# Optimization experiments

Measured on AMD Instinct MI355X. Metric: run time of the kernel, lower is better.

## Reference

```python
import jax, jax.numpy as jnp
import numpy as np
from jax import lax

B, T, J, C = 256, 512, 25, 3
IN_DIM = J * C  # 75
H = 256


def gru_layer(x, W_ih, W_hh, b_ih, b_hh):
    """PyTorch-semantics GRU layer. x: [B,T,Din] -> (out [B,T,H], h_T [B,H]).
    Gate order in stacked weights: r, z, n (PyTorch convention)."""
    Hh = W_hh.shape[1]
    # precompute input contributions for all timesteps
    xg = jnp.einsum('bti,gi->btg', x, W_ih) + b_ih  # [B,T,3H]

    def step(h, xg_t):
        hg = h @ W_hh.T + b_hh  # [B,3H]
        xr, xz, xn = jnp.split(xg_t, 3, axis=-1)
        hr, hz, hn = jnp.split(hg, 3, axis=-1)
        r = jax.nn.sigmoid(xr + hr)
        z = jax.nn.sigmoid(xz + hz)
        n = jnp.tanh(xn + r * hn)
        h_new = (1.0 - z) * n + z * h
        return h_new, h_new

    h0 = jnp.zeros((x.shape[0], Hh), x.dtype)
    hT, outs = lax.scan(step, h0, jnp.swapaxes(xg, 0, 1))  # scan over time
    return jnp.swapaxes(outs, 0, 1), hT


def setup_inputs() -> dict:
    key = jax.random.key(0)
    ks = jax.random.split(key, 12)
    s_in = 1.0 / np.sqrt(H)

    def u(k, shape):
        return jax.random.uniform(k, shape, jnp.float32, -s_in, s_in)

    return {
        'x': jax.random.normal(ks[0], (B, T, J, C), jnp.float32),
        'W_ih0': u(ks[1], (3 * H, IN_DIM)),
        'W_hh0': u(ks[2], (3 * H, H)),
        'b_ih0': u(ks[3], (3 * H,)),
        'b_hh0': u(ks[4], (3 * H,)),
        'W_ih1': u(ks[5], (3 * H, H)),
        'W_hh1': u(ks[6], (3 * H, H)),
        'b_ih1': u(ks[7], (3 * H,)),
        'b_hh1': u(ks[8], (3 * H,)),
        'fc_W': u(ks[9], (H, H)),
        'fc_b': u(ks[10], (H,)),
    }


def reference(x, W_ih0, W_hh0, b_ih0, b_hh0, W_ih1, W_hh1, b_ih1, b_hh1, fc_W, fc_b):
    b, t, j, c = x.shape
    xf = x.reshape(b, t, j * 3)  # matches torch view(B, T, J*3)
    out0, _ = gru_layer(xf, W_ih0, W_hh0, b_ih0, b_hh0)
    _, hT = gru_layer(out0, W_ih1, W_hh1, b_ih1, b_hh1)
    # unidirectional: final hidden state of last layer -> fc
    embedding = hT @ fc_W.T + fc_b  # [B, H]
    return embedding
```

## Files before the change

kernel.cpp:

```cpp
#include <hip/hip_runtime.h>
#include <hip/hip_bf16.h>
#include <stdint.h>
#include <stddef.h>


typedef _Float16 f16;
typedef _Float16 f16x8 __attribute__((ext_vector_type(8)));
typedef _Float16 f16x4 __attribute__((ext_vector_type(4)));
typedef float    f32x4 __attribute__((ext_vector_type(4)));

#define B_      256
#define T_      512
#define H_      256
#define G_      768
#define IN_RAW  75
#define KX      96
#define MROWS   (T_*B_)

__device__ __forceinline__ float rcp_(float x){ return __builtin_amdgcn_rcpf(x); }
__device__ __forceinline__ float sigm(float x){ return rcp_(1.f + __expf(-x)); }
__device__ __forceinline__ float tanh_(float x){ return 1.f - 2.f*rcp_(1.f + __expf(2.f*x)); }

__device__ __forceinline__ void bar_lds(){
  asm volatile("s_waitcnt lgkmcnt(0)" ::: "memory");
  __builtin_amdgcn_s_barrier();
  __builtin_amdgcn_sched_barrier(0);
}

__global__ __launch_bounds__(256) void cast_x(const float* __restrict__ x,
                                              f16* __restrict__ xb){
  int idx = blockIdx.x*256 + threadIdx.x;
  int row = idx / KX;
  int j   = idx - row*KX;
  int t   = row >> 8;
  int b   = row & 255;
  float v = (j < IN_RAW) ? x[((size_t)b*T_ + t)*IN_RAW + j] : 0.f;
  xb[idx] = (f16)v;
}

__global__ __launch_bounds__(256) void cast_w(
    const float* __restrict__ Wih0, const float* __restrict__ Whh0,
    const float* __restrict__ Wih1, const float* __restrict__ Whh1,
    const float* __restrict__ fcW,
    const float* __restrict__ bih0, const float* __restrict__ bhh0,
    const float* __restrict__ bih1, const float* __restrict__ bhh1,
    f16* __restrict__ W0h, f16* __restrict__ Whh0h, f16* __restrict__ Wih1h,
    f16* __restrict__ Whh1h, f16* __restrict__ fcWh,
    float* __restrict__ bias0, float* __restrict__ bias1){
  int i = blockIdx.x*256 + threadIdx.x;
  if (i < 73728){ int r = i/KX, j = i - r*KX;
    W0h[i] = (f16)((j < IN_RAW) ? Wih0[r*IN_RAW + j] : 0.f); return; }
  i -= 73728;
  if (i < 196608){ Whh0h[i] = (f16)Whh0[i]; return; } i -= 196608;
  if (i < 196608){ Wih1h[i] = (f16)Wih1[i]; return; } i -= 196608;
  if (i < 196608){ Whh1h[i] = (f16)Whh1[i]; return; } i -= 196608;
  if (i < 65536){ fcWh[i] = (f16)fcW[i]; return; } i -= 65536;
  if (i < 768){ bias0[i] = bih0[i] + (i < 512 ? bhh0[i] : 0.f); return; } i -= 768;
  if (i < 768){ bias1[i] = bih1[i] + (i < 512 ? bhh1[i] : 0.f); }
}

__global__ __launch_bounds__(256) void cast_h(const float* __restrict__ hs,
                                              f16* __restrict__ hT){
  int i = blockIdx.x*256 + threadIdx.x;
  hT[i] = (f16)hs[i];
}

template<int K, int BN, bool OUTF32>
__global__ __launch_bounds__(256, 2) void gemm_k(const f16* __restrict__ A,
    const f16* __restrict__ W, const float* __restrict__ bias,
    void* __restrict__ outp, const int N){
  constexpr int NT = BN/16;
  const int tid  = threadIdx.x;
  const int wave = tid >> 6, lane = tid & 63;
  const int quad = lane >> 4, l16 = lane & 15;
  const long mbase = (long)blockIdx.x*128 + wave*32;
  const int  nbase = blockIdx.y*BN;
  f32x4 acc[2][NT] = {};
#pragma unroll 2
  for (int kc = 0; kc < K/32; ++kc){
    f16x8 a0 = *(const f16x8*)(A + (mbase +      l16)*K + kc*32 + quad*8);
    f16x8 a1 = *(const f16x8*)(A + (mbase + 16 + l16)*K + kc*32 + quad*8);
#pragma unroll
    for (int nt = 0; nt < NT; ++nt){
      f16x8 b = *(const f16x8*)(W + (long)(nbase + nt*16 + l16)*K + kc*32 + quad*8);
      acc[0][nt] = __builtin_amdgcn_mfma_f32_16x16x32_f16(a0, b, acc[0][nt], 0, 0, 0);
      acc[1][nt] = __builtin_amdgcn_mfma_f32_16x16x32_f16(a1, b, acc[1][nt], 0, 0, 0);
    }
  }
#pragma unroll
  for (int nt = 0; nt < NT; ++nt){
    const int col = nbase + nt*16 + l16;
    const float bv = bias[col];
#pragma unroll
    for (int af = 0; af < 2; ++af){
#pragma unroll
      for (int r = 0; r < 4; ++r){
        const long row = mbase + af*16 + quad*4 + r;
        float v = acc[af][nt][r] + bv;
        if (OUTF32) ((float*)outp)[row*(long)N + col] = v;
        else        ((f16*)outp)[row*(long)N + col] = (f16)v;
      }
    }
  }
}

template<int K>
__device__ __forceinline__ void gemm_body128(const f16* __restrict__ A,
    const f16* __restrict__ W, const float* __restrict__ bias,
    f16* __restrict__ out, const int bx, const int by){
  const int tid  = threadIdx.x;
  const int wave = tid >> 6, lane = tid & 63;
  const int quad = lane >> 4, l16 = lane & 15;
  const int nbase = by*128;
#pragma unroll
  for (int mt = 0; mt < 2; ++mt){
    const long mbase = (long)bx*512 + mt*256 + wave*32;
    f32x4 acc[2][8] = {};
#pragma unroll 2
    for (int kc = 0; kc < K/32; ++kc){
      f16x8 a0 = *(const f16x8*)(A + (mbase +      l16)*K + kc*32 + quad*8);
      f16x8 a1 = *(const f16x8*)(A + (mbase + 16 + l16)*K + kc*32 + quad*8);
#pragma unroll
      for (int nt = 0; nt < 8; ++nt){
        f16x8 b = *(const f16x8*)(W + (long)(nbase + nt*16 + l16)*K + kc*32 + quad*8);
        acc[0][nt] = __builtin_amdgcn_mfma_f32_16x16x32_f16(a0, b, acc[0][nt], 0, 0, 0);
        acc[1][nt] = __builtin_amdgcn_mfma_f32_16x16x32_f16(a1, b, acc[1][nt], 0, 0, 0);
      }
    }
#pragma unroll
    for (int nt = 0; nt < 8; ++nt){
      const int col = nbase + nt*16 + l16;
      const float bv = bias[col];
#pragma unroll
      for (int af = 0; af < 2; ++af)
#pragma unroll
        for (int r = 0; r < 4; ++r)
          out[(mbase + af*16 + quad*4 + r)*(long)G_ + col] = (f16)(acc[af][nt][r] + bv);
    }
  }
}

__device__ __forceinline__ void scan_body(const f16* __restrict__ xg,
    const f16* __restrict__ Whh, const float* __restrict__ bhh,
    float* __restrict__ hstate, f16* __restrict__ out0,
    const int TC, const int bx){
  __shared__ char  hbufB[2][16*512];
  __shared__ f16   nlds[65536];
  __shared__ float bnlds[256];
  const int tid  = threadIdx.x;
  const int wave = tid >> 6, lane = tid & 63;
  const int quad = lane >> 4, l16 = lane & 15;
  const int b0   = bx*16;
  const int jj   = wave*32 + quad*4;

  f16x8 w[2][2][8];
#pragma unroll
  for (int s = 0; s < 2; ++s)
#pragma unroll
    for (int g = 0; g < 2; ++g)
#pragma unroll
      for (int kc = 0; kc < 8; ++kc)
        w[s][g][kc] = *(const f16x8*)(Whh + (size_t)(g*256 + wave*32 + s*16 + l16)*H_ + kc*32 + quad*8);
#pragma unroll
  for (int s = 0; s < 2; ++s)
#pragma unroll
    for (int g = 0; g < 2; ++g)
#pragma unroll
      for (int kc = 0; kc < 8; ++kc)
        asm volatile("" : "+a"(w[s][g][kc]));

#pragma unroll
  for (int i = 0; i < 16; ++i){
    const int p  = i*512 + tid;
    const int f  = p >> 6, L = p & 63;
    const int wv = f >> 4, ss = (f >> 3) & 1, kcc = f & 7;
    const int row = 512 + wv*32 + ss*16 + (L & 15);
    const int k   = kcc*32 + (L >> 4)*8;
    *(f16x8*)&nlds[(size_t)p*8] = *(const f16x8*)(Whh + (size_t)row*H_ + k);
  }
  if (tid < 256) bnlds[tid] = bhh[512 + tid];

  f32x4 h[2];
#pragma unroll
  for (int s = 0; s < 2; ++s){
    h[s] = *(const f32x4*)(hstate + (size_t)(b0 + l16)*H_ + jj + s*16);
    f16x4 hh;
#pragma unroll
    for (int r = 0; r < 4; ++r) hh[r] = (f16)h[s][r];
    const int ch = wave*4 + s*2 + (quad>>1);
    *(f16x4*)&hbufB[0][l16*512 + ((ch ^ (l16&7))<<4) + ((quad&1)<<3)] = hh;
  }

  const f16* xgl = xg + (size_t)(b0 + l16)*G_ + jj;
  f16x4 cur[6];
#pragma unroll
  for (int s = 0; s < 2; ++s)
#pragma unroll
    for (int g = 0; g < 3; ++g)
      cur[s*3+g] = *(const f16x4*)(xgl + g*256 + s*16);

  __syncthreads();

  for (int t = 0; t < TC; ++t){
    const int pb = t & 1;
    f32x4 acc[2][3] = {};
#pragma unroll
    for (int kc = 0; kc < 8; ++kc){
      f16x8 hf = *(const f16x8*)&hbufB[pb][l16*512 + ((((kc<<2)|quad) ^ (l16&7))<<4)];
#pragma unroll
      for (int s = 0; s < 2; ++s){
        acc[s][0] = __builtin_amdgcn_mfma_f32_16x16x32_f16(w[s][0][kc], hf, acc[s][0], 0,0,0);
        acc[s][1] = __builtin_amdgcn_mfma_f32_16x16x32_f16(w[s][1][kc], hf, acc[s][1], 0,0,0);
        f16x8 nf = *(const f16x8*)&nlds[(size_t)(((wave<<4)|(s<<3)|kc)*64 + lane)*8];
        acc[s][2] = __builtin_amdgcn_mfma_f32_16x16x32_f16(nf, hf, acc[s][2], 0,0,0);
      }
    }
    f16x4 hh[2];
#pragma unroll
    for (int s = 0; s < 2; ++s){
      const f32x4 bnv = *(const f32x4*)&bnlds[jj + s*16];
#pragma unroll
      for (int r = 0; r < 4; ++r){
        float rg = sigm((float)cur[s*3+0][r] + acc[s][0][r]);
        float zg = sigm((float)cur[s*3+1][r] + acc[s][1][r]);
        float ng = tanh_((float)cur[s*3+2][r] + rg*(acc[s][2][r] + bnv[r]));
        float hv = (1.f - zg)*ng + zg*h[s][r];
        h[s][r] = hv;
        hh[s][r] = (f16)hv;
      }
    }
    if (t+1 < TC){
      const f16* xn_ = xgl + (size_t)(t+1)*(B_*G_);
#pragma unroll
      for (int s = 0; s < 2; ++s)
#pragma unroll
        for (int g = 0; g < 3; ++g)
          cur[s*3+g] = *(const f16x4*)(xn_ + g*256 + s*16);
    }
#pragma unroll
    for (int s = 0; s < 2; ++s){
      const int ch = wave*4 + s*2 + (quad>>1);
      *(f16x4*)&hbufB[pb^1][l16*512 + ((ch ^ (l16&7))<<4) + ((quad&1)<<3)] = hh[s];
      if (out0)
        *(f16x4*)(out0 + ((size_t)t*B_ + b0 + l16)*H_ + jj + s*16) = hh[s];
    }
    bar_lds();
  }

#pragma unroll
  for (int s = 0; s < 2; ++s)
    *(f32x4*)(hstate + (size_t)(b0 + l16)*H_ + jj + s*16) = h[s];
}

__global__ __launch_bounds__(512)
__attribute__((amdgpu_waves_per_eu(2, 2)))
void fused(
    const f16* __restrict__ xg0, const f16* __restrict__ Whh0,
    const float* __restrict__ bhh0, float* __restrict__ h0s,
    f16* __restrict__ out0w,
    const f16* __restrict__ xg1, const f16* __restrict__ Whh1,
    const float* __restrict__ bhh1, float* __restrict__ h1s,
    const f16* __restrict__ g0A, const f16* __restrict__ g0W,
    const float* __restrict__ g0b, f16* __restrict__ g0out,
    const f16* __restrict__ g1A, const f16* __restrict__ g1W,
    const float* __restrict__ g1b, f16* __restrict__ g1out,
    const int TC, const int mask){
  const int bid = blockIdx.x;
  if (bid < 16){
    if (!(mask & 1)) return;
    scan_body(xg0, Whh0, bhh0, h0s, out0w, TC, bid);
  } else if (bid < 32){
    if (!(mask & 2)) return;
    scan_body(xg1, Whh1, bhh1, h1s, (f16*)nullptr, TC, bid - 16);
  } else {
    int g = bid - 32;
    const int RB = TC/2;
    if (g < 3*TC){
      if (!(mask & 4)) return;
      gemm_body128<96>(g0A, g0W, g0b, g0out, g % RB, g / RB);
    } else {
      g -= 3*TC;
      if (!(mask & 8)) return;
      gemm_body128<256>(g1A, g1W, g1b, g1out, g % RB, g / RB);
    }
  }
}

extern "C" void kernel_launch(void* const* d_in, const int* in_sizes, int n_in,
                              void* d_out, int out_size, void* d_ws, size_t ws_size,
                              hipStream_t stream){
  (void)in_sizes; (void)n_in; (void)out_size;
  const float* x    = (const float*)d_in[0];
  const float* Wih0 = (const float*)d_in[1];
  const float* Whh0 = (const float*)d_in[2];
  const float* bih0 = (const float*)d_in[3];
  const float* bhh0 = (const float*)d_in[4];
  const float* Wih1 = (const float*)d_in[5];
  const float* Whh1 = (const float*)d_in[6];
  const float* bih1 = (const float*)d_in[7];
  const float* bhh1 = (const float*)d_in[8];
  const float* fcW  = (const float*)d_in[9];
  const float* fcb  = (const float*)d_in[10];

  char* ws = (char*)d_ws;
  size_t off = 0;
  auto alloc = [&](size_t bytes) -> void* {
    void* p = ws + off; off += (bytes + 255) & ~(size_t)255; return p;
  };
  f16*   xb    = (f16*)  alloc((size_t)MROWS*KX*2);
  f16*   W0h   = (f16*)  alloc((size_t)G_*KX*2);
  f16*   Whh0h = (f16*)  alloc((size_t)G_*H_*2);
  f16*   Wih1h = (f16*)  alloc((size_t)G_*H_*2);
  f16*   Whh1h = (f16*)  alloc((size_t)G_*H_*2);
  f16*   fcWh  = (f16*)  alloc((size_t)H_*H_*2);
  float* bias0 = (float*)alloc(G_*4);
  float* bias1 = (float*)alloc(G_*4);
  float* h0s   = (float*)alloc((size_t)B_*H_*4);
  float* h1s   = (float*)alloc((size_t)B_*H_*4);
  f16*   hTh   = (f16*)  alloc((size_t)B_*H_*2);
  const size_t fixed = off;

  int TC = 32;
  while (TC > 8 && fixed + (size_t)TC*1835008 + 1024 > ws_size) TC >>= 1;
  f16* xg0[2], *xg1[2], *out0[2];
  xg0[0]  = (f16*)alloc((size_t)TC*B_*G_*2);
  xg0[1]  = (f16*)alloc((size_t)TC*B_*G_*2);
  xg1[0]  = (f16*)alloc((size_t)TC*B_*G_*2);
  xg1[1]  = (f16*)alloc((size_t)TC*B_*G_*2);
  out0[0] = (f16*)alloc((size_t)TC*B_*H_*2);
  out0[1] = (f16*)alloc((size_t)TC*B_*H_*2);
  const int nc = T_ / TC;

  hipMemsetAsync(h0s, 0, (size_t)B_*H_*4*2, stream);
  hipLaunchKernelGGL(cast_x, dim3(49152), dim3(256), 0, stream, x, xb);
  hipLaunchKernelGGL(cast_w, dim3(2854), dim3(256), 0, stream,
                     Wih0, Whh0, Wih1, Whh1, fcW, bih0, bhh0, bih1, bhh1,
                     W0h, Whh0h, Wih1h, Whh1h, fcWh, bias0, bias1);

  hipLaunchKernelGGL((gemm_k<96,192,false>), dim3(TC*2,4), dim3(256), 0, stream,
                     xb, W0h, bias0, (void*)xg0[0], G_);

  const dim3 grid(32 + 6*TC);
  for (int i = 0; i <= nc + 1; ++i){
    int mask = 0;
    if (i < nc)            mask |= 1;
    if (i >= 2)            mask |= 2;
    if (i + 1 < nc)        mask |= 4;
    if (i >= 1 && i <= nc) mask |= 8;
    hipLaunchKernelGGL(fused, grid, dim3(512), 0, stream,
                       xg0[i&1], Whh0h, bhh0, h0s, out0[i&1],
                       xg1[i&1], Whh1h, bhh1, h1s,
                       xb + (size_t)(i+1)*TC*B_*KX, W0h, bias0, xg0[(i+1)&1],
                       out0[(i+1)&1], Wih1h, bias1, xg1[(i+1)&1],
                       TC, mask);
  }

  hipLaunchKernelGGL(cast_h, dim3(256), dim3(256), 0, stream, h1s, hTh);
  hipLaunchKernelGGL((gemm_k<256,64,true>), dim3(2,4), dim3(256), 0, stream,
                     hTh, fcWh, fcb, d_out, H_);
}
```

Measured before the change: 1.688 ms.

## Hold all recurrent weights in registers with 4-wave scan blocks

```diff
diff --git a/kernel.cpp b/kernel.cpp
--- a/kernel.cpp
+++ b/kernel.cpp
@@ -105,30 +105,30 @@
 }
 
 template<int K>
-__device__ __forceinline__ void gemm_body128(const f16* __restrict__ A,
+__device__ __forceinline__ void gemm_body4(const f16* __restrict__ A,
     const f16* __restrict__ W, const float* __restrict__ bias,
     f16* __restrict__ out, const int bx, const int by){
   const int tid  = threadIdx.x;
   const int wave = tid >> 6, lane = tid & 63;
   const int quad = lane >> 4, l16 = lane & 15;
-  const int nbase = by*128;
+  const int nbase = by*384;
 #pragma unroll
   for (int mt = 0; mt < 2; ++mt){
-    const long mbase = (long)bx*512 + mt*256 + wave*32;
-    f32x4 acc[2][8] = {};
-#pragma unroll 2
+    const long mbase = (long)bx*256 + mt*128 + wave*32;
+    f32x4 acc[2][24] = {};
+#pragma unroll 1
     for (int kc = 0; kc < K/32; ++kc){
       f16x8 a0 = *(const f16x8*)(A + (mbase +      l16)*K + kc*32 + quad*8);
       f16x8 a1 = *(const f16x8*)(A + (mbase + 16 + l16)*K + kc*32 + quad*8);
 #pragma unroll
-      for (int nt = 0; nt < 8; ++nt){
+      for (int nt = 0; nt < 24; ++nt){
         f16x8 b = *(const f16x8*)(W + (long)(nbase + nt*16 + l16)*K + kc*32 + quad*8);
         acc[0][nt] = __builtin_amdgcn_mfma_f32_16x16x32_f16(a0, b, acc[0][nt], 0, 0, 0);
         acc[1][nt] = __builtin_amdgcn_mfma_f32_16x16x32_f16(a1, b, acc[1][nt], 0, 0, 0);
       }
     }
 #pragma unroll
-    for (int nt = 0; nt < 8; ++nt){
+    for (int nt = 0; nt < 24; ++nt){
       const int col = nbase + nt*16 + l16;
       const float bv = bias[col];
 #pragma unroll
@@ -144,116 +144,111 @@
     const f16* __restrict__ Whh, const float* __restrict__ bhh,
     float* __restrict__ hstate, f16* __restrict__ out0,
     const int TC, const int bx){
-  __shared__ char  hbufB[2][16*512];
-  __shared__ f16   nlds[65536];
+  __shared__ char  hbufB[2][8192];
   __shared__ float bnlds[256];
   const int tid  = threadIdx.x;
   const int wave = tid >> 6, lane = tid & 63;
   const int quad = lane >> 4, l16 = lane & 15;
   const int b0   = bx*16;
-  const int jj   = wave*32 + quad*4;
-
-  f16x8 w[2][2][8];
-#pragma unroll
-  for (int s = 0; s < 2; ++s)
-#pragma unroll
-    for (int g = 0; g < 2; ++g)
-#pragma unroll
-      for (int kc = 0; kc < 8; ++kc)
-        w[s][g][kc] = *(const f16x8*)(Whh + (size_t)(g*256 + wave*32 + s*16 + l16)*H_ + kc*32 + quad*8);
-#pragma unroll
-  for (int s = 0; s < 2; ++s)
-#pragma unroll
-    for (int g = 0; g < 2; ++g)
-#pragma unroll
-      for (int kc = 0; kc < 8; ++kc)
-        asm volatile("" : "+a"(w[s][g][kc]));
-
-#pragma unroll
-  for (int i = 0; i < 16; ++i){
-    const int p  = i*512 + tid;
-    const int f  = p >> 6, L = p & 63;
-    const int wv = f >> 4, ss = (f >> 3) & 1, kcc = f & 7;
-    const int row = 512 + wv*32 + ss*16 + (L & 15);
-    const int k   = kcc*32 + (L >> 4)*8;
-    *(f16x8*)&nlds[(size_t)p*8] = *(const f16x8*)(Whh + (size_t)row*H_ + k);
-  }
-  if (tid < 256) bnlds[tid] = bhh[512 + tid];
-
-  f32x4 h[2];
-#pragma unroll
-  for (int s = 0; s < 2; ++s){
+  const int jj   = wave*64 + quad*4;
+
+  f16x8 wz[4][8], wn[4][8], wr[4][8];
+#pragma unroll
+  for (int s = 0; s < 4; ++s)
+#pragma unroll
+    for (int kc = 0; kc < 8; ++kc){
+      wz[s][kc] = *(const f16x8*)(Whh + (size_t)(256 + wave*64 + s*16 + l16)*H_ + kc*32 + quad*8);
+      asm volatile("" : "+a"(wz[s][kc]));
+    }
+#pragma unroll
+  for (int s = 0; s < 4; ++s)
+#pragma unroll
+    for (int kc = 0; kc < 8; ++kc){
+      wn[s][kc] = *(const f16x8*)(Whh + (size_t)(512 + wave*64 + s*16 + l16)*H_ + kc*32 + quad*8);
+      asm volatile("" : "+a"(wn[s][kc]));
+    }
+#pragma unroll
+  for (int s = 0; s < 4; ++s)
+#pragma unroll
+    for (int kc = 0; kc < 8; ++kc){
+      wr[s][kc] = *(const f16x8*)(Whh + (size_t)(wave*64 + s*16 + l16)*H_ + kc*32 + quad*8);
+      asm volatile("" : "+v"(wr[s][kc]));
+    }
+
+  bnlds[tid] = bhh[512 + tid];
+
+  f32x4 h[4];
+#pragma unroll
+  for (int s = 0; s < 4; ++s){
     h[s] = *(const f32x4*)(hstate + (size_t)(b0 + l16)*H_ + jj + s*16);
     f16x4 hh;
 #pragma unroll
     for (int r = 0; r < 4; ++r) hh[r] = (f16)h[s][r];
-    const int ch = wave*4 + s*2 + (quad>>1);
+    const int ch = wave*8 + s*2 + (quad>>1);
     *(f16x4*)&hbufB[0][l16*512 + ((ch ^ (l16&7))<<4) + ((quad&1)<<3)] = hh;
   }
 
   const f16* xgl = xg + (size_t)(b0 + l16)*G_ + jj;
-  f16x4 cur[6];
-#pragma unroll
-  for (int s = 0; s < 2; ++s)
+  f16* o0l = out0 ? out0 + (size_t)(b0 + l16)*H_ + jj : (f16*)nullptr;
+  f16x4 cur[12];
+#pragma unroll
+  for (int s = 0; s < 4; ++s)
 #pragma unroll
     for (int g = 0; g < 3; ++g)
       cur[s*3+g] = *(const f16x4*)(xgl + g*256 + s*16);
 
   __syncthreads();
 
+#pragma unroll 1
   for (int t = 0; t < TC; ++t){
     const int pb = t & 1;
-    f32x4 acc[2][3] = {};
+    f32x4 accR[4] = {}, accZ[4] = {}, accN[4] = {};
 #pragma unroll
     for (int kc = 0; kc < 8; ++kc){
       f16x8 hf = *(const f16x8*)&hbufB[pb][l16*512 + ((((kc<<2)|quad) ^ (l16&7))<<4)];
 #pragma unroll
-      for (int s = 0; s < 2; ++s){
-        acc[s][0] = __builtin_amdgcn_mfma_f32_16x16x32_f16(w[s][0][kc], hf, acc[s][0], 0,0,0);
-        acc[s][1] = __builtin_amdgcn_mfma_f32_16x16x32_f16(w[s][1][kc], hf, acc[s][1], 0,0,0);
-        f16x8 nf = *(const f16x8*)&nlds[(size_t)(((wave<<4)|(s<<3)|kc)*64 + lane)*8];
-        acc[s][2] = __builtin_amdgcn_mfma_f32_16x16x32_f16(nf, hf, acc[s][2], 0,0,0);
+      for (int s = 0; s < 4; ++s){
+        accR[s] = __builtin_amdgcn_mfma_f32_16x16x32_f16(wr[s][kc], hf, accR[s], 0,0,0);
+        accZ[s] = __builtin_amdgcn_mfma_f32_16x16x32_f16(wz[s][kc], hf, accZ[s], 0,0,0);
+        accN[s] = __builtin_amdgcn_mfma_f32_16x16x32_f16(wn[s][kc], hf, accN[s], 0,0,0);
       }
     }
-    f16x4 hh[2];
-#pragma unroll
-    for (int s = 0; s < 2; ++s){
+#pragma unroll
+    for (int s = 0; s < 4; ++s){
       const f32x4 bnv = *(const f32x4*)&bnlds[jj + s*16];
+      f16x4 hh;
 #pragma unroll
       for (int r = 0; r < 4; ++r){
-        float rg = sigm((float)cur[s*3+0][r] + acc[s][0][r]);
-        float zg = sigm((float)cur[s*3+1][r] + acc[s][1][r]);
-        float ng = tanh_((float)cur[s*3+2][r] + rg*(acc[s][2][r] + bnv[r]));
-        float hv = (1.f - zg)*ng + zg*h[s][r];
+        float rg = sigm((float)cur[s*3+0][r] + accR[s][r]);
+        float zg = sigm((float)cur[s*3+1][r] + accZ[s][r]);
+        float ng = tanh_((float)cur[s*3+2][r] + rg*(accN[s][r] + bnv[r]));
+        float hv = ng + zg*(h[s][r] - ng);
         h[s][r] = hv;
-        hh[s][r] = (f16)hv;
+        hh[r]   = (f16)hv;
       }
+      const int ch = wave*8 + s*2 + (quad>>1);
+      *(f16x4*)&hbufB[pb^1][l16*512 + ((ch ^ (l16&7))<<4) + ((quad&1)<<3)] = hh;
+      if (o0l)
+        *(f16x4*)(o0l + (size_t)t*(B_*H_) + s*16) = hh;
     }
     if (t+1 < TC){
       const f16* xn_ = xgl + (size_t)(t+1)*(B_*G_);
 #pragma unroll
-      for (int s = 0; s < 2; ++s)
+      for (int s = 0; s < 4; ++s)
 #pragma unroll
         for (int g = 0; g < 3; ++g)
           cur[s*3+g] = *(const f16x4*)(xn_ + g*256 + s*16);
     }
-#pragma unroll
-    for (int s = 0; s < 2; ++s){
-      const int ch = wave*4 + s*2 + (quad>>1);
-      *(f16x4*)&hbufB[pb^1][l16*512 + ((ch ^ (l16&7))<<4) + ((quad&1)<<3)] = hh[s];
-      if (out0)
-        *(f16x4*)(out0 + ((size_t)t*B_ + b0 + l16)*H_ + jj + s*16) = hh[s];
-    }
     bar_lds();
   }
 
 #pragma unroll
-  for (int s = 0; s < 2; ++s)
+  for (int s = 0; s < 4; ++s)
     *(f32x4*)(hstate + (size_t)(b0 + l16)*H_ + jj + s*16) = h[s];
 }
 
-__global__ __launch_bounds__(512)
-__attribute__((amdgpu_waves_per_eu(2, 2)))
+__global__ __launch_bounds__(256, 1)
+__attribute__((amdgpu_waves_per_eu(1, 1)))
 void fused(
     const f16* __restrict__ xg0, const f16* __restrict__ Whh0,
     const float* __restrict__ bhh0, float* __restrict__ h0s,
@@ -274,14 +269,13 @@
     scan_body(xg1, Whh1, bhh1, h1s, (f16*)nullptr, TC, bid - 16);
   } else {
     int g = bid - 32;
-    const int RB = TC/2;
-    if (g < 3*TC){
+    if (g < 2*TC){
       if (!(mask & 4)) return;
-      gemm_body128<96>(g0A, g0W, g0b, g0out, g % RB, g / RB);
+      gemm_body4<96>(g0A, g0W, g0b, g0out, g % TC, g / TC);
     } else {
-      g -= 3*TC;
+      g -= 2*TC;
       if (!(mask & 8)) return;
-      gemm_body128<256>(g1A, g1W, g1b, g1out, g % RB, g / RB);
+      gemm_body4<256>(g1A, g1W, g1b, g1out, g % TC, g / TC);
     }
   }
 }
@@ -340,14 +334,14 @@
   hipLaunchKernelGGL((gemm_k<96,192,false>), dim3(TC*2,4), dim3(256), 0, stream,
                      xb, W0h, bias0, (void*)xg0[0], G_);
 
-  const dim3 grid(32 + 6*TC);
+  const dim3 grid(32 + 4*TC);
   for (int i = 0; i <= nc + 1; ++i){
     int mask = 0;
     if (i < nc)            mask |= 1;
     if (i >= 2)            mask |= 2;
     if (i + 1 < nc)        mask |= 4;
     if (i >= 1 && i <= nc) mask |= 8;
-    hipLaunchKernelGGL(fused, grid, dim3(512), 0, stream,
+    hipLaunchKernelGGL(fused, grid, dim3(256), 0, stream,
                        xg0[i&1], Whh0h, bhh0, h0s, out0[i&1],
                        xg1[i&1], Whh1h, bhh1, h1s,
                        xb + (size_t)(i+1)*TC*B_*KX, W0h, bias0, xg0[(i+1)&1],
```

Result: slower. 2.816 ms (+66.9%).

## Replace per-chunk kernel launches with one persistent cooperative kernel using grid sync

Applied to the files above, without the earlier changes.

```diff
diff --git a/kernel.cpp b/kernel.cpp
--- a/kernel.cpp
+++ b/kernel.cpp
@@ -1,7 +1,10 @@
 #include <hip/hip_runtime.h>
 #include <hip/hip_bf16.h>
+#include <hip/hip_cooperative_groups.h>
 #include <stdint.h>
 #include <stddef.h>
+
+namespace cg = cooperative_groups;
 
 
 typedef _Float16 f16;
@@ -144,7 +147,7 @@
     const f16* __restrict__ Whh, const float* __restrict__ bhh,
     float* __restrict__ hstate, f16* __restrict__ out0,
     const int TC, const int bx){
-  __shared__ char  hbufB[2][16*512];
+  __shared__ char  hbufB[2][8192];
   __shared__ f16   nlds[65536];
   __shared__ float bnlds[256];
   const int tid  = threadIdx.x;
@@ -286,6 +289,156 @@
   }
 }
 
+__global__ __launch_bounds__(512)
+__attribute__((amdgpu_waves_per_eu(2, 2)))
+void fusedP(const f16* __restrict__ xb,
+            const f16* __restrict__ W0h, const float* __restrict__ bias0,
+            const f16* __restrict__ Whh0h, const float* __restrict__ bhh0,
+            const f16* __restrict__ Wih1h, const float* __restrict__ bias1,
+            const f16* __restrict__ Whh1h, const float* __restrict__ bhh1,
+            float* __restrict__ h1s,
+            f16* __restrict__ xg0a, f16* __restrict__ xg0b,
+            f16* __restrict__ xg1a, f16* __restrict__ xg1b,
+            f16* __restrict__ out0a, f16* __restrict__ out0b,
+            const int TC, const int nc){
+  cg::grid_group gg = cg::this_grid();
+  const int bid = blockIdx.x;
+  if (bid < 32){
+    __shared__ char  hbufB[2][8192];
+    __shared__ f16   nlds[65536];
+    __shared__ float bnlds[256];
+    const bool L1w = bid >= 16;
+    const f16*   Whh = L1w ? Whh1h : Whh0h;
+    const float* bhh = L1w ? bhh1  : bhh0;
+    const int tid  = threadIdx.x;
+    const int wave = tid >> 6, lane = tid & 63;
+    const int quad = lane >> 4, l16 = lane & 15;
+    const int b0   = (bid & 15)*16;
+    const int jj   = wave*32 + quad*4;
+
+    f16x8 w[2][2][8];
+#pragma unroll
+    for (int s = 0; s < 2; ++s)
+#pragma unroll
+      for (int g = 0; g < 2; ++g)
+#pragma unroll
+        for (int kc = 0; kc < 8; ++kc)
+          w[s][g][kc] = *(const f16x8*)(Whh + (size_t)(g*256 + wave*32 + s*16 + l16)*H_ + kc*32 + quad*8);
+#pragma unroll
+    for (int s = 0; s < 2; ++s)
+#pragma unroll
+      for (int g = 0; g < 2; ++g)
+#pragma unroll
+        for (int kc = 0; kc < 8; ++kc)
+          asm volatile("" : "+a"(w[s][g][kc]));
+
+#pragma unroll
+    for (int i = 0; i < 16; ++i){
+      const int p  = i*512 + tid;
+      const int f  = p >> 6, L = p & 63;
+      const int wv = f >> 4, ss = (f >> 3) & 1, kcc = f & 7;
+      const int row = 512 + wv*32 + ss*16 + (L & 15);
+      const int k   = kcc*32 + (L >> 4)*8;
+      *(f16x8*)&nlds[(size_t)p*8] = *(const f16x8*)(Whh + (size_t)row*H_ + k);
+    }
+    if (tid < 256) bnlds[tid] = bhh[512 + tid];
+
+    f32x4 h[2] = {};
+#pragma unroll
+    for (int s = 0; s < 2; ++s){
+      const int ch = wave*4 + s*2 + (quad>>1);
+      *(f16x4*)&hbufB[0][l16*512 + ((ch ^ (l16&7))<<4) + ((quad&1)<<3)] = (f16x4){0,0,0,0};
+    }
+    __syncthreads();
+
+    for (int i = 0; i <= nc + 1; ++i){
+      const int c = L1w ? i - 2 : i;
+      if (c >= 0 && c < nc){
+        const f16* xgc = L1w ? ((c&1) ? xg1b : xg1a) : ((c&1) ? xg0b : xg0a);
+        f16* o0c       = L1w ? (f16*)nullptr        : ((c&1) ? out0b : out0a);
+        const f16* xgl = xgc + (size_t)(b0 + l16)*G_ + jj;
+        f16* o0l = o0c ? o0c + (size_t)(b0 + l16)*H_ + jj : (f16*)nullptr;
+        f16x4 cur[6];
+#pragma unroll
+        for (int s = 0; s < 2; ++s)
+#pragma unroll
+          for (int g = 0; g < 3; ++g)
+            cur[s*3+g] = *(const f16x4*)(xgl + g*256 + s*16);
+
+        for (int t = 0; t < TC; ++t){
+          const int pb = t & 1;
+          f32x4 acc[2][3] = {};
+#pragma unroll
+          for (int kc = 0; kc < 8; ++kc){
+            f16x8 hf = *(const f16x8*)&hbufB[pb][l16*512 + ((((kc<<2)|quad) ^ (l16&7))<<4)];
+#pragma unroll
+            for (int s = 0; s < 2; ++s){
+              acc[s][0] = __builtin_amdgcn_mfma_f32_16x16x32_f16(w[s][0][kc], hf, acc[s][0], 0,0,0);
+              acc[s][1] = __builtin_amdgcn_mfma_f32_16x16x32_f16(w[s][1][kc], hf, acc[s][1], 0,0,0);
+              f16x8 nf = *(const f16x8*)&nlds[(size_t)(((wave<<4)|(s<<3)|kc)*64 + lane)*8];
+              acc[s][2] = __builtin_amdgcn_mfma_f32_16x16x32_f16(nf, hf, acc[s][2], 0,0,0);
+            }
+          }
+          f16x4 hh[2];
+#pragma unroll
+          for (int s = 0; s < 2; ++s){
+            const f32x4 bnv = *(const f32x4*)&bnlds[jj + s*16];
+#pragma unroll
+            for (int r = 0; r < 4; ++r){
+              float rg = sigm((float)cur[s*3+0][r] + acc[s][0][r]);
+              float zg = sigm((float)cur[s*3+1][r] + acc[s][1][r]);
+              float ng = tanh_((float)cur[s*3+2][r] + rg*(acc[s][2][r] + bnv[r]));
+              float hv = (1.f - zg)*ng + zg*h[s][r];
+              h[s][r] = hv;
+              hh[s][r] = (f16)hv;
+            }
+          }
+          if (t+1 < TC){
+            const f16* xn_ = xgl + (size_t)(t+1)*(B_*G_);
+#pragma unroll
+            for (int s = 0; s < 2; ++s)
+#pragma unroll
+              for (int g = 0; g < 3; ++g)
+                cur[s*3+g] = *(const f16x4*)(xn_ + g*256 + s*16);
+          }
+#pragma unroll
+          for (int s = 0; s < 2; ++s){
+            const int ch = wave*4 + s*2 + (quad>>1);
+            *(f16x4*)&hbufB[pb^1][l16*512 + ((ch ^ (l16&7))<<4) + ((quad&1)<<3)] = hh[s];
+            if (o0l)
+              *(f16x4*)(o0l + (size_t)t*(B_*H_) + s*16) = hh[s];
+          }
+          bar_lds();
+        }
+      }
+      __threadfence();
+      gg.sync();
+    }
+    if (L1w){
+#pragma unroll
+      for (int s = 0; s < 2; ++s)
+        *(f32x4*)(h1s + (size_t)(b0 + l16)*H_ + jj + s*16) = h[s];
+    }
+  } else {
+    const int g0 = bid - 32;
+    const int RB = TC/2;
+    for (int i = 0; i <= nc + 1; ++i){
+      if (g0 < 3*TC){
+        if (i + 1 < nc)
+          gemm_body128<96>(xb + (size_t)(i+1)*TC*B_*KX, W0h, bias0,
+                           ((i+1)&1) ? xg0b : xg0a, g0 % RB, g0 / RB);
+      } else {
+        const int g1 = g0 - 3*TC;
+        if (i >= 1 && i <= nc)
+          gemm_body128<256>(((i+1)&1) ? out0b : out0a, Wih1h, bias1,
+                            ((i+1)&1) ? xg1b : xg1a, g1 % RB, g1 / RB);
+      }
+      __threadfence();
+      gg.sync();
+    }
+  }
+}
+
 extern "C" void kernel_launch(void* const* d_in, const int* in_sizes, int n_in,
                               void* d_out, int out_size, void* d_ws, size_t ws_size,
                               hipStream_t stream){
@@ -340,19 +493,34 @@
   hipLaunchKernelGGL((gemm_k<96,192,false>), dim3(TC*2,4), dim3(256), 0, stream,
                      xb, W0h, bias0, (void*)xg0[0], G_);
 
-  const dim3 grid(32 + 6*TC);
-  for (int i = 0; i <= nc + 1; ++i){
-    int mask = 0;
-    if (i < nc)            mask |= 1;
-    if (i >= 2)            mask |= 2;
-    if (i + 1 < nc)        mask |= 4;
-    if (i >= 1 && i <= nc) mask |= 8;
-    hipLaunchKernelGGL(fused, grid, dim3(512), 0, stream,
-                       xg0[i&1], Whh0h, bhh0, h0s, out0[i&1],
-                       xg1[i&1], Whh1h, bhh1, h1s,
-                       xb + (size_t)(i+1)*TC*B_*KX, W0h, bias0, xg0[(i+1)&1],
-                       out0[(i+1)&1], Wih1h, bias1, xg1[(i+1)&1],
-                       TC, mask);
+  {
+    const f16* xb_ = xb; const f16* W0h_ = W0h; const float* b0_ = bias0;
+    const f16* Wh0_ = Whh0h; const float* bh0_ = bhh0;
+    const f16* Wi1_ = Wih1h; const float* b1_ = bias1;
+    const f16* Wh1_ = Whh1h; const float* bh1_ = bhh1;
+    float* h1s_ = h1s;
+    f16 *x0a = xg0[0], *x0b = xg0[1], *x1a = xg1[0], *x1b = xg1[1];
+    f16 *o0a = out0[0], *o0b = out0[1];
+    int TC_ = TC, nc_ = nc;
+    void* kargs[] = { &xb_, &W0h_, &b0_, &Wh0_, &bh0_, &Wi1_, &b1_, &Wh1_, &bh1_,
+                      &h1s_, &x0a, &x0b, &x1a, &x1b, &o0a, &o0b, &TC_, &nc_ };
+    hipError_t e = hipLaunchCooperativeKernel((void*)fusedP, dim3(32 + 6*TC),
+                                              dim3(512), kargs, 0, stream);
+    if (e != hipSuccess){
+      for (int i = 0; i <= nc + 1; ++i){
+        int mask = 0;
+        if (i < nc)            mask |= 1;
+        if (i >= 2)            mask |= 2;
+        if (i + 1 < nc)        mask |= 4;
+        if (i >= 1 && i <= nc) mask |= 8;
+        hipLaunchKernelGGL(fused, dim3(32 + 6*TC), dim3(512), 0, stream,
+                           xg0[i&1], Whh0h, bhh0, h0s, out0[i&1],
+                           xg1[i&1], Whh1h, bhh1, h1s,
+                           xb + (size_t)(i+1)*TC*B_*KX, W0h, bias0, xg0[(i+1)&1],
+                           out0[(i+1)&1], Wih1h, bias1, xg1[(i+1)&1],
+                           TC, mask);
+      }
+    }
   }
 
   hipLaunchKernelGGL(cast_h, dim3(256), dim3(256), 0, stream, h1s, hTh);
```

Result: slower. 2.646 ms (+56.8%).
